# Kernel optimization log

Hardware: AMD Instinct MI355X
Metric: run time of the kernel (lower is better)

The kernel has to match this reference:

```python
import jax, jax.numpy as jnp
import numpy as np

B, Q, K, D, H = 16, 128, 128, 512, 512
NEG = -1e6


def setup_inputs() -> dict:
    key = jax.random.key(0)
    ks = jax.random.split(key, 7)
    return {
        "queries": jax.random.normal(ks[0], (B, Q, D), dtype=jnp.float32),
        "keys": jax.random.normal(ks[1], (B, K, D), dtype=jnp.float32),
        "values": jax.random.normal(ks[2], (B, K, D), dtype=jnp.float32),
        "valid_lens": jax.random.randint(ks[3], (B,), 1, K + 1, dtype=jnp.int32),
        "Wq": jax.random.normal(ks[4], (D, H), dtype=jnp.float32) / np.sqrt(D),
        "Wk": jax.random.normal(ks[5], (D, H), dtype=jnp.float32) / np.sqrt(D),
        "wv": jax.random.normal(ks[6], (H,), dtype=jnp.float32) / np.sqrt(H),
    }


def reference(queries, keys, values, valid_lens, Wq, Wk, wv):
    # projections (LazyLinear, bias=False)
    q = jnp.einsum("bqd,dh->bqh", queries, Wq)  # [B,Q,H]
    k = jnp.einsum("bkd,dh->bkh", keys, Wk)    # [B,K,H]
    # broadcast add -> tanh -> reduce to scalar score (Bahdanau)
    feats = jnp.tanh(q[:, :, None, :] + k[:, None, :, :])  # [B,Q,K,H]
    scores = jnp.einsum("bqkh,h->bqk", feats, wv)           # [B,Q,K]
    # masked softmax over key dim using per-batch valid lengths
    mask = jnp.arange(scores.shape[-1])[None, None, :] < valid_lens[:, None, None]
    scores = jnp.where(mask, scores, NEG)
    attn = jax.nn.softmax(scores, axis=-1)                  # [B,Q,K]
    # dropout is identity in eval mode
    return jnp.einsum("bqk,bkv->bqv", attn, values)
```

## Files before the change

kernel.cpp:

```cpp
#include <hip/hip_runtime.h>

#define Bn 16
#define Qn 128
#define Kn 128
#define Dn 512
#define Hn 512
#define NEGV (-3.0e38f)
#define PSCALE 2.8853900817779268f

typedef short s16x8 __attribute__((ext_vector_type(8)));
typedef float f32x4 __attribute__((ext_vector_type(4)));

__device__ __forceinline__ float exp2_hw(float x) {
  float r;
  asm("v_exp_f32 %0, %1" : "=v"(r) : "v"(x));
  return r;
}
__device__ __forceinline__ float rcp_hw(float x) { return __builtin_amdgcn_rcpf(x); }
__device__ __forceinline__ unsigned short f2bf(float f) {
  unsigned int u = __float_as_uint(f);
  u += 0x7fff + ((u >> 16) & 1);
  return (unsigned short)(u >> 16);
}
__device__ __forceinline__ unsigned int pack2bf(float lo, float hi) {
  return (unsigned int)f2bf(lo) | ((unsigned int)f2bf(hi) << 16);
}
__device__ __forceinline__ float bfl(unsigned int u) { return __uint_as_float(u << 16); }
__device__ __forceinline__ float bfh(unsigned int u) { return __uint_as_float(u & 0xffff0000u); }

__global__ __launch_bounds__(256) void convert_w(
    const float* __restrict__ Wq, const float* __restrict__ Wk,
    unsigned short* __restrict__ Wt)
{
  __shared__ float Tl[64][68];
  const int bid = blockIdx.x, t = threadIdx.x;
  const int sel = bid >> 6, tile = bid & 63;
  const int kt = tile >> 3, nt = tile & 7;
  const float* W = sel ? Wk : Wq;

  const int r0 = t >> 4, c4 = (t & 15) * 4;
  #pragma unroll
  for (int p = 0; p < 4; ++p) {
    int r = r0 + p * 16;
    float4 v = *(const float4*)(W + (size_t)(kt * 64 + r) * Hn + nt * 64 + c4);
    *(float4*)&Tl[r][c4] = v;
  }
  __syncthreads();

  const int n_l = t >> 3, k8 = (t & 7) * 8;
  #pragma unroll
  for (int p = 0; p < 2; ++p) {
    int n = n_l + p * 32;
    unsigned short o[8];
    #pragma unroll
    for (int i = 0; i < 8; ++i) o[i] = f2bf(Tl[k8 + i][n]);
    unsigned short* dst = Wt + (size_t)sel * 262144 + (size_t)(nt * 64 + n) * 512 + kt * 64 + k8;
    *(ushort4*)dst = *(const ushort4*)&o[0];
    *(ushort4*)(dst + 4) = *(const ushort4*)&o[4];
  }
}

__global__ __launch_bounds__(256) void proj_mfma(
    const float* __restrict__ queries, const float* __restrict__ keys,
    const unsigned short* __restrict__ Wt, const float* __restrict__ wv,
    unsigned int* __restrict__ QWp, unsigned int* __restrict__ Ekp)
{
  __shared__ unsigned short Al[64][72];
  __shared__ unsigned short Bl[128][72];
  __shared__ float Tep[64][68];
  const int t = threadIdx.x, w = t >> 6, l = t & 63;
  const int wm = w >> 1, wn = w & 1;
  const int rowTile = blockIdx.x;
  const int n0 = blockIdx.y * 128;
  const int R0 = rowTile * 64;
  const bool isQ = rowTile < 32;
  const float* Asrc = isQ ? queries : keys;
  const int rowBase = isQ ? R0 : (R0 - 2048);
  const unsigned short* Wsel = Wt + (isQ ? 0 : 262144);

  f32x4 acc[2][4];
  #pragma unroll
  for (int m = 0; m < 2; ++m)
    #pragma unroll
    for (int n = 0; n < 4; ++n) acc[m][n] = (f32x4)0.f;

  const int lr = l & 15, lk = l >> 4;

  for (int k0 = 0; k0 < Hn; k0 += 64) {
    float4 afr[4];
    ushort4 br[4][2];
    #pragma unroll
    for (int i = 0; i < 4; ++i) {
      int g = t + 256 * i, r = g >> 4, c4 = g & 15;
      afr[i] = *(const float4*)(Asrc + (size_t)(rowBase + r) * Dn + k0 + c4 * 4);
    }
    #pragma unroll
    for (int i = 0; i < 4; ++i) {
      int g = t + 256 * i, r = g >> 3, c = g & 7;
      const unsigned short* p = Wsel + (size_t)(n0 + r) * Hn + k0 + c * 8;
      br[i][0] = *(const ushort4*)p; br[i][1] = *(const ushort4*)(p + 4);
    }
    __syncthreads();
    #pragma unroll
    for (int i = 0; i < 4; ++i) {
      int g = t + 256 * i, r = g >> 4, c4 = g & 15;
      ushort4 o = {f2bf(afr[i].x), f2bf(afr[i].y), f2bf(afr[i].z), f2bf(afr[i].w)};
      *(ushort4*)&Al[r][c4 * 4] = o;
    }
    #pragma unroll
    for (int i = 0; i < 4; ++i) {
      int g = t + 256 * i, r = g >> 3, c = g & 7;
      *(ushort4*)&Bl[r][c * 8] = br[i][0]; *(ushort4*)&Bl[r][c * 8 + 4] = br[i][1];
    }
    __syncthreads();
    #pragma unroll
    for (int ks = 0; ks < 2; ++ks) {
      s16x8 af[2], bf_[4];
      #pragma unroll
      for (int m = 0; m < 2; ++m)
        af[m] = *(const s16x8*)&Al[wm * 32 + m * 16 + lr][ks * 32 + lk * 8];
      #pragma unroll
      for (int n = 0; n < 4; ++n)
        bf_[n] = *(const s16x8*)&Bl[wn * 64 + n * 16 + lr][ks * 32 + lk * 8];
      #pragma unroll
      for (int m = 0; m < 2; ++m)
        #pragma unroll
        for (int n = 0; n < 4; ++n)
          acc[m][n] = __builtin_amdgcn_mfma_f32_16x16x32_bf16(af[m], bf_[n], acc[m][n], 0, 0, 0);
    }
    __syncthreads();
  }

  if (isQ) {
    #pragma unroll
    for (int m = 0; m < 2; ++m)
      #pragma unroll
      for (int n = 0; n < 4; ++n)
        #pragma unroll
        for (int r = 0; r < 4; ++r) {
          int row = R0 + wm * 32 + m * 16 + lk * 4 + r;
          int col = n0 + wn * 64 + n * 16 + lr;
          float a = acc[m][n][r];
          float F  = exp2_hw(-PSCALE * a);
          float WF = -2.f * wv[col] * F;
          QWp[(size_t)row * Hn + col] = pack2bf(WF, F);
        }
  } else {
    const int krow0 = R0 - 2048;
    const int bb = krow0 >> 7, kb = krow0 & 127;
    const int hl = t >> 2, kq = (t & 3) * 16;
    #pragma unroll
    for (int hc = 0; hc < 2; ++hc) {
      __syncthreads();
      if (wn == hc) {
        #pragma unroll
        for (int m = 0; m < 2; ++m)
          #pragma unroll
          for (int n = 0; n < 4; ++n)
            #pragma unroll
            for (int r = 0; r < 4; ++r) {
              int row_l = wm * 32 + m * 16 + lk * 4 + r;
              int h_l = n * 16 + lr;
              Tep[h_l][row_l] = exp2_hw(PSCALE * acc[m][n][r]);
            }
      }
      __syncthreads();
      unsigned int* dst = Ekp + (size_t)bb * 32768
                        + (size_t)(n0 + hc * 64 + hl) * 64 + (kb + kq) / 2;
      #pragma unroll
      for (int j = 0; j < 4; ++j) {
        float4 v = *(const float4*)&Tep[hl][kq + j * 4];
        uint2 o = {pack2bf(v.x, v.y), pack2bf(v.z, v.w)};
        *(uint2*)(dst + j * 2) = o;
      }
    }
  }
}

__device__ __forceinline__ void term8(float WF0, float F0, float WF1, float F1,
                                      const float ek0[8], const float ek1[8],
                                      float acc[8]) {
  #pragma unroll
  for (int j = 0; j < 8; ++j) {
    float d0 = F0 + ek0[j];
    float d1 = F1 + ek1[j];
    float num = __builtin_fmaf(WF0, d1, WF1 * d0);
    acc[j] = __builtin_fmaf(num, rcp_hw(d0 * d1), acc[j]);
  }
}

__global__ __launch_bounds__(256) void score_kernel(
    const unsigned int* __restrict__ QWp, const unsigned int* __restrict__ Ekp,
    float* __restrict__ Sp)
{
  __shared__ float EkL[64][128];
  __shared__ unsigned int QWLu[32][68];
  const int id = blockIdx.x;
  const int g = id & 127, qt = id >> 7;
  const int b = g >> 3, hs = g & 7;
  const int t = threadIdx.x, w = t >> 6, l = t & 63;
  const int qp = w * 8 + ((l >> 4) << 1);
  const int ka8 = (l & 15) * 8;

  {
    const uint4* esrc = (const uint4*)(Ekp + (size_t)b * 32768 + (size_t)hs * 4096);
    uint4 er[4];
    #pragma unroll
    for (int i = 0; i < 4; ++i) er[i] = esrc[t + 256 * i];
    uint4 qr[2];
    #pragma unroll
    for (int i = 0; i < 2; ++i) {
      int lin = t + 256 * i, row = lin >> 4, c4 = lin & 15;
      qr[i] = *(const uint4*)(QWp + (size_t)(b * Qn + qt * 32 + row) * Hn + hs * 64 + c4 * 4);
    }
    #pragma unroll
    for (int i = 0; i < 4; ++i) {
      int lin = t + 256 * i, row = lin >> 4, c4 = lin & 15;
      const unsigned int u[4] = {er[i].x, er[i].y, er[i].z, er[i].w};
      float f[8];
      #pragma unroll
      for (int p = 0; p < 4; ++p) { f[2 * p] = bfl(u[p]); f[2 * p + 1] = bfh(u[p]); }
      *(float4*)&EkL[row][c4 * 8]     = *(const float4*)&f[0];
      *(float4*)&EkL[row][c4 * 8 + 4] = *(const float4*)&f[4];
    }
    #pragma unroll
    for (int i = 0; i < 2; ++i) {
      int lin = t + 256 * i, row = lin >> 4, c4 = lin & 15;
      *(uint4*)&QWLu[row][c4 * 4] = qr[i];
    }
  }
  __syncthreads();

  float acc0[8], acc1[8];
  #pragma unroll
  for (int j = 0; j < 8; ++j) { acc0[j] = 0.f; acc1[j] = 0.f; }

  #pragma unroll 4
  for (int hb = 0; hb < 32; ++hb) {
    float ek0[8], ek1[8];
    *(float4*)&ek0[0] = *(const float4*)&EkL[2 * hb][ka8];
    *(float4*)&ek0[4] = *(const float4*)&EkL[2 * hb][ka8 + 4];
    *(float4*)&ek1[0] = *(const float4*)&EkL[2 * hb + 1][ka8];
    *(float4*)&ek1[4] = *(const float4*)&EkL[2 * hb + 1][ka8 + 4];
    uint2 qa = *(const uint2*)&QWLu[qp][hb * 2];
    uint2 qb = *(const uint2*)&QWLu[qp + 1][hb * 2];
    term8(bfl(qa.x), bfh(qa.x), bfl(qa.y), bfh(qa.y), ek0, ek1, acc0);
    term8(bfl(qb.x), bfh(qb.x), bfl(qb.y), bfh(qb.y), ek0, ek1, acc1);
  }

  const int q = qt * 32 + qp;
  size_t sb = (((size_t)hs * Bn + b) * Qn + q) * Kn;
  *(float4*)(Sp + sb + ka8)          = (float4){acc0[0], acc0[1], acc0[2], acc0[3]};
  *(float4*)(Sp + sb + ka8 + 4)      = (float4){acc0[4], acc0[5], acc0[6], acc0[7]};
  *(float4*)(Sp + sb + Kn + ka8)     = (float4){acc1[0], acc1[1], acc1[2], acc1[3]};
  *(float4*)(Sp + sb + Kn + ka8 + 4) = (float4){acc1[4], acc1[5], acc1[6], acc1[7]};
}

__global__ __launch_bounds__(256) void softmax_av(
    const float* __restrict__ Sp, const int* __restrict__ valid_lens,
    const float* __restrict__ values, float* __restrict__ out)
{
  __shared__ unsigned short AtL[16][136];
  __shared__ unsigned int VLu[128][36];
  const int t = threadIdx.x, w = t >> 6, l = t & 63;
  const int b = blockIdx.y;
  const int qt = blockIdx.x & 7;
  const int dt = blockIdx.x >> 3;
  const int lr = l & 15, lk = l >> 4;

  {
    const int q_l = t >> 4, k8 = (t & 15) * 8;
    const size_t base = ((size_t)(b * Qn) + qt * 16 + q_l) * Kn + k8;
    float s[8] = {0.f, 0.f, 0.f, 0.f, 0.f, 0.f, 0.f, 0.f};
    #pragma unroll
    for (int p = 0; p < 8; ++p) {
      float4 a0 = *(const float4*)(Sp + base + (size_t)p * 262144);
      float4 a1 = *(const float4*)(Sp + base + (size_t)p * 262144 + 4);
      s[0] += a0.x; s[1] += a0.y; s[2] += a0.z; s[3] += a0.w;
      s[4] += a1.x; s[5] += a1.y; s[6] += a1.z; s[7] += a1.w;
    }
    const int vlen = valid_lens[b];
    bool ok[8];
    float m = NEGV;
    #pragma unroll
    for (int j = 0; j < 8; ++j) {
      ok[j] = (k8 + j) < vlen;
      if (ok[j]) m = fmaxf(m, s[j]);
    }
    #pragma unroll
    for (int xm = 8; xm >= 1; xm >>= 1) m = fmaxf(m, __shfl_xor(m, xm));
    float e[8], sum = 0.f;
    #pragma unroll
    for (int j = 0; j < 8; ++j) {
      e[j] = ok[j] ? exp2_hw((s[j] - m) * 1.44269504f) : 0.f;
      sum += e[j];
    }
    #pragma unroll
    for (int xm = 8; xm >= 1; xm >>= 1) sum += __shfl_xor(sum, xm);
    float inv = rcp_hw(sum);
    ushort4 o0 = {f2bf(e[0] * inv), f2bf(e[1] * inv), f2bf(e[2] * inv), f2bf(e[3] * inv)};
    ushort4 o1 = {f2bf(e[4] * inv), f2bf(e[5] * inv), f2bf(e[6] * inv), f2bf(e[7] * inv)};
    *(ushort4*)&AtL[q_l][k8] = o0;
    *(ushort4*)&AtL[q_l][k8 + 4] = o1;
  }
  __syncthreads();

  const int kread = t & 15, dread = (t >> 4) & 15;
  f32x4 acc[2];
  acc[0] = (f32x4)0.f; acc[1] = (f32x4)0.f;
  #pragma unroll
  for (int k0 = 0; k0 < Kn; k0 += 64) {
    if (k0) __syncthreads();
    #pragma unroll
    for (int j = 0; j < 4; ++j) {
      int k2 = kread + 16 * (j & 1);
      int d4 = dread + 16 * (j >> 1);
      const float* vp = values + ((size_t)(b * Kn) + k0 + 2 * k2) * Dn + dt * 128 + d4 * 4;
      float4 v0 = *(const float4*)(vp);
      float4 v1 = *(const float4*)(vp + Dn);
      VLu[d4 * 4 + 0][k2] = pack2bf(v0.x, v1.x);
      VLu[d4 * 4 + 1][k2] = pack2bf(v0.y, v1.y);
      VLu[d4 * 4 + 2][k2] = pack2bf(v0.z, v1.z);
      VLu[d4 * 4 + 3][k2] = pack2bf(v0.w, v1.w);
    }
    __syncthreads();
    #pragma unroll
    for (int ks = 0; ks < 2; ++ks) {
      s16x8 af = *(const s16x8*)&AtL[lr][k0 + ks * 32 + lk * 8];
      #pragma unroll
      for (int nn = 0; nn < 2; ++nn) {
        s16x8 bv = *(const s16x8*)&VLu[w * 32 + nn * 16 + lr][ks * 16 + lk * 4];
        acc[nn] = __builtin_amdgcn_mfma_f32_16x16x32_bf16(af, bv, acc[nn], 0, 0, 0);
      }
    }
  }
  #pragma unroll
  for (int nn = 0; nn < 2; ++nn)
    #pragma unroll
    for (int r = 0; r < 4; ++r) {
      int q = qt * 16 + lk * 4 + r;
      int d = dt * 128 + w * 32 + nn * 16 + lr;
      out[((size_t)(b * Qn) + q) * Dn + d] = acc[nn][r];
    }
}

extern "C" void kernel_launch(void* const* d_in, const int* in_sizes, int n_in,
                              void* d_out, int out_size, void* d_ws, size_t ws_size,
                              hipStream_t stream) {
  const float* queries    = (const float*)d_in[0];
  const float* keys       = (const float*)d_in[1];
  const float* values     = (const float*)d_in[2];
  const int*   valid_lens = (const int*)d_in[3];
  const float* Wq         = (const float*)d_in[4];
  const float* Wk         = (const float*)d_in[5];
  const float* wv         = (const float*)d_in[6];
  float* out = (float*)d_out;

  unsigned short* Wt  = (unsigned short*)d_ws;
  unsigned int*   QWp = (unsigned int*)(Wt + 524288);
  unsigned int*   Ekp = QWp + 1048576;
  float*          Sp  = (float*)(Ekp + 524288);

  convert_w<<<128, 256, 0, stream>>>(Wq, Wk, Wt);
  proj_mfma<<<dim3(64, 4), 256, 0, stream>>>(queries, keys, Wt, wv, QWp, Ekp);
  score_kernel<<<512, 256, 0, stream>>>(QWp, Ekp, Sp);
  softmax_av<<<dim3(32, 16), 256, 0, stream>>>(Sp, valid_lens, values, out);
}
```

Before: 46.19 us.

## Fuse score computation with masked softmax and attention-value matmul

Merges score_kernel and softmax_av into one kernel in which each 512-thread block handles 8 queries of one batch. The block loops over all 8 H-slices to accumulate full scores in registers, runs the softmax with wave-level shuffles, and feeds the probabilities to the MFMA value product. This removes the partial-score buffer written to global memory, its re-read, and one launch. In exchange there are only 256 blocks, each looping serially over H, half of every MFMA tile is zero padding, and each block re-reads Ek and the values tiles for its batch.

```diff
diff --git a/kernel.cpp b/kernel.cpp
--- a/kernel.cpp
+++ b/kernel.cpp
@@ -177,171 +177,122 @@
   }
 }
 
-__device__ __forceinline__ void term8(float WF0, float F0, float WF1, float F1,
-                                      const float ek0[8], const float ek1[8],
-                                      float acc[8]) {
-  #pragma unroll
-  for (int j = 0; j < 8; ++j) {
-    float d0 = F0 + ek0[j];
-    float d1 = F1 + ek1[j];
-    float num = __builtin_fmaf(WF0, d1, WF1 * d0);
-    acc[j] = __builtin_fmaf(num, rcp_hw(d0 * d1), acc[j]);
-  }
-}
-
-__global__ __launch_bounds__(256) void score_kernel(
+__global__ __launch_bounds__(512) void fused_sav(
     const unsigned int* __restrict__ QWp, const unsigned int* __restrict__ Ekp,
-    float* __restrict__ Sp)
+    const int* __restrict__ valid_lens, const float* __restrict__ values,
+    float* __restrict__ out)
 {
-  __shared__ float EkL[64][128];
-  __shared__ unsigned int QWLu[32][68];
+  __shared__ union {
+    struct { float EkL[64][128]; unsigned int QWLu[8][512]; } s;
+    struct { unsigned short AtL[16][136]; unsigned int VLu[128][36]; } a;
+  } sm;
   const int id = blockIdx.x;
-  const int g = id & 127, qt = id >> 7;
-  const int b = g >> 3, hs = g & 7;
-  const int t = threadIdx.x, w = t >> 6, l = t & 63;
-  const int qp = w * 8 + ((l >> 4) << 1);
-  const int ka8 = (l & 15) * 8;
-
-  {
-    const uint4* esrc = (const uint4*)(Ekp + (size_t)b * 32768 + (size_t)hs * 4096);
-    uint4 er[4];
-    #pragma unroll
-    for (int i = 0; i < 4; ++i) er[i] = esrc[t + 256 * i];
-    uint4 qr[2];
-    #pragma unroll
-    for (int i = 0; i < 2; ++i) {
-      int lin = t + 256 * i, row = lin >> 4, c4 = lin & 15;
-      qr[i] = *(const uint4*)(QWp + (size_t)(b * Qn + qt * 32 + row) * Hn + hs * 64 + c4 * 4);
-    }
-    #pragma unroll
-    for (int i = 0; i < 4; ++i) {
-      int lin = t + 256 * i, row = lin >> 4, c4 = lin & 15;
-      const unsigned int u[4] = {er[i].x, er[i].y, er[i].z, er[i].w};
-      float f[8];
-      #pragma unroll
-      for (int p = 0; p < 4; ++p) { f[2 * p] = bfl(u[p]); f[2 * p + 1] = bfh(u[p]); }
-      *(float4*)&EkL[row][c4 * 8]     = *(const float4*)&f[0];
-      *(float4*)&EkL[row][c4 * 8 + 4] = *(const float4*)&f[4];
-    }
-    #pragma unroll
-    for (int i = 0; i < 2; ++i) {
-      int lin = t + 256 * i, row = lin >> 4, c4 = lin & 15;
-      *(uint4*)&QWLu[row][c4 * 4] = qr[i];
-    }
-  }
+  const int b  = ((id & 7) << 1) | (id >> 7);
+  const int qt = (id >> 3) & 15;
+  const int t = threadIdx.x, l = t & 63, wq = t >> 6;
+  const int k2 = l * 2;
+  const int lr = l & 15, lk = l >> 4;
+
+  #pragma unroll
+  for (int i = 0; i < 2; ++i) {
+    int lin = t + 512 * i;
+    int row = lin >> 7, c4 = lin & 127;
+    uint4 v = *(const uint4*)(QWp + (size_t)(b * Qn + qt * 8 + row) * Hn + c4 * 4);
+    *(uint4*)&sm.s.QWLu[row][c4 * 4] = v;
+  }
+
+  float acc0 = 0.f, acc1 = 0.f;
+  for (int hs = 0; hs < 8; ++hs) {
+    __syncthreads();
+    {
+      const uint4* esrc = (const uint4*)(Ekp + (size_t)b * 32768 + (size_t)hs * 4096);
+      #pragma unroll
+      for (int i = 0; i < 2; ++i) {
+        int lin = t + 512 * i;
+        uint4 e = esrc[lin];
+        int row = lin >> 4, c4 = lin & 15;
+        const unsigned int u[4] = {e.x, e.y, e.z, e.w};
+        float f[8];
+        #pragma unroll
+        for (int p = 0; p < 4; ++p) { f[2 * p] = bfl(u[p]); f[2 * p + 1] = bfh(u[p]); }
+        *(float4*)&sm.s.EkL[row][c4 * 8]     = *(const float4*)&f[0];
+        *(float4*)&sm.s.EkL[row][c4 * 8 + 4] = *(const float4*)&f[4];
+      }
+    }
+    __syncthreads();
+    const unsigned int* qrow = &sm.s.QWLu[wq][hs * 64];
+    #pragma unroll 4
+    for (int hb = 0; hb < 32; ++hb) {
+      float2 e0 = *(const float2*)&sm.s.EkL[2 * hb][k2];
+      float2 e1 = *(const float2*)&sm.s.EkL[2 * hb + 1][k2];
+      uint2 qa = *(const uint2*)&qrow[hb * 2];
+      const float WF0 = bfl(qa.x), F0 = bfh(qa.x);
+      const float WF1 = bfl(qa.y), F1 = bfh(qa.y);
+      float d0, d1, num;
+      d0 = F0 + e0.x; d1 = F1 + e1.x;
+      num = __builtin_fmaf(WF0, d1, WF1 * d0);
+      acc0 = __builtin_fmaf(num, rcp_hw(d0 * d1), acc0);
+      d0 = F0 + e0.y; d1 = F1 + e1.y;
+      num = __builtin_fmaf(WF0, d1, WF1 * d0);
+      acc1 = __builtin_fmaf(num, rcp_hw(d0 * d1), acc1);
+    }
+  }
+
+  const int vlen = valid_lens[b];
+  const bool ok0 = k2 < vlen, ok1 = (k2 + 1) < vlen;
+  float m = fmaxf(ok0 ? acc0 : NEGV, ok1 ? acc1 : NEGV);
+  #pragma unroll
+  for (int xm = 32; xm >= 1; xm >>= 1) m = fmaxf(m, __shfl_xor(m, xm));
+  float e0v = ok0 ? exp2_hw((acc0 - m) * 1.44269504f) : 0.f;
+  float e1v = ok1 ? exp2_hw((acc1 - m) * 1.44269504f) : 0.f;
+  float ssum = e0v + e1v;
+  #pragma unroll
+  for (int xm = 32; xm >= 1; xm >>= 1) ssum += __shfl_xor(ssum, xm);
+  float inv = rcp_hw(ssum);
+
   __syncthreads();
-
-  float acc0[8], acc1[8];
-  #pragma unroll
-  for (int j = 0; j < 8; ++j) { acc0[j] = 0.f; acc1[j] = 0.f; }
-
-  #pragma unroll 4
-  for (int hb = 0; hb < 32; ++hb) {
-    float ek0[8], ek1[8];
-    *(float4*)&ek0[0] = *(const float4*)&EkL[2 * hb][ka8];
-    *(float4*)&ek0[4] = *(const float4*)&EkL[2 * hb][ka8 + 4];
-    *(float4*)&ek1[0] = *(const float4*)&EkL[2 * hb + 1][ka8];
-    *(float4*)&ek1[4] = *(const float4*)&EkL[2 * hb + 1][ka8 + 4];
-    uint2 qa = *(const uint2*)&QWLu[qp][hb * 2];
-    uint2 qb = *(const uint2*)&QWLu[qp + 1][hb * 2];
-    term8(bfl(qa.x), bfh(qa.x), bfl(qa.y), bfh(qa.y), ek0, ek1, acc0);
-    term8(bfl(qb.x), bfh(qb.x), bfl(qb.y), bfh(qb.y), ek0, ek1, acc1);
-  }
-
-  const int q = qt * 32 + qp;
-  size_t sb = (((size_t)hs * Bn + b) * Qn + q) * Kn;
-  *(float4*)(Sp + sb + ka8)          = (float4){acc0[0], acc0[1], acc0[2], acc0[3]};
-  *(float4*)(Sp + sb + ka8 + 4)      = (float4){acc0[4], acc0[5], acc0[6], acc0[7]};
-  *(float4*)(Sp + sb + Kn + ka8)     = (float4){acc1[0], acc1[1], acc1[2], acc1[3]};
-  *(float4*)(Sp + sb + Kn + ka8 + 4) = (float4){acc1[4], acc1[5], acc1[6], acc1[7]};
-}
-
-__global__ __launch_bounds__(256) void softmax_av(
-    const float* __restrict__ Sp, const int* __restrict__ valid_lens,
-    const float* __restrict__ values, float* __restrict__ out)
-{
-  __shared__ unsigned short AtL[16][136];
-  __shared__ unsigned int VLu[128][36];
-  const int t = threadIdx.x, w = t >> 6, l = t & 63;
-  const int b = blockIdx.y;
-  const int qt = blockIdx.x & 7;
-  const int dt = blockIdx.x >> 3;
-  const int lr = l & 15, lk = l >> 4;
-
-  {
-    const int q_l = t >> 4, k8 = (t & 15) * 8;
-    const size_t base = ((size_t)(b * Qn) + qt * 16 + q_l) * Kn + k8;
-    float s[8] = {0.f, 0.f, 0.f, 0.f, 0.f, 0.f, 0.f, 0.f};
-    #pragma unroll
-    for (int p = 0; p < 8; ++p) {
-      float4 a0 = *(const float4*)(Sp + base + (size_t)p * 262144);
-      float4 a1 = *(const float4*)(Sp + base + (size_t)p * 262144 + 4);
-      s[0] += a0.x; s[1] += a0.y; s[2] += a0.z; s[3] += a0.w;
-      s[4] += a1.x; s[5] += a1.y; s[6] += a1.z; s[7] += a1.w;
-    }
-    const int vlen = valid_lens[b];
-    bool ok[8];
-    float m = NEGV;
-    #pragma unroll
-    for (int j = 0; j < 8; ++j) {
-      ok[j] = (k8 + j) < vlen;
-      if (ok[j]) m = fmaxf(m, s[j]);
-    }
-    #pragma unroll
-    for (int xm = 8; xm >= 1; xm >>= 1) m = fmaxf(m, __shfl_xor(m, xm));
-    float e[8], sum = 0.f;
-    #pragma unroll
-    for (int j = 0; j < 8; ++j) {
-      e[j] = ok[j] ? exp2_hw((s[j] - m) * 1.44269504f) : 0.f;
-      sum += e[j];
-    }
-    #pragma unroll
-    for (int xm = 8; xm >= 1; xm >>= 1) sum += __shfl_xor(sum, xm);
-    float inv = rcp_hw(sum);
-    ushort4 o0 = {f2bf(e[0] * inv), f2bf(e[1] * inv), f2bf(e[2] * inv), f2bf(e[3] * inv)};
-    ushort4 o1 = {f2bf(e[4] * inv), f2bf(e[5] * inv), f2bf(e[6] * inv), f2bf(e[7] * inv)};
-    *(ushort4*)&AtL[q_l][k8] = o0;
-    *(ushort4*)&AtL[q_l][k8 + 4] = o1;
-  }
-  __syncthreads();
-
-  const int kread = t & 15, dread = (t >> 4) & 15;
-  f32x4 acc[2];
-  acc[0] = (f32x4)0.f; acc[1] = (f32x4)0.f;
-  #pragma unroll
-  for (int k0 = 0; k0 < Kn; k0 += 64) {
-    if (k0) __syncthreads();
-    #pragma unroll
-    for (int j = 0; j < 4; ++j) {
-      int k2 = kread + 16 * (j & 1);
-      int d4 = dread + 16 * (j >> 1);
-      const float* vp = values + ((size_t)(b * Kn) + k0 + 2 * k2) * Dn + dt * 128 + d4 * 4;
-      float4 v0 = *(const float4*)(vp);
-      float4 v1 = *(const float4*)(vp + Dn);
-      VLu[d4 * 4 + 0][k2] = pack2bf(v0.x, v1.x);
-      VLu[d4 * 4 + 1][k2] = pack2bf(v0.y, v1.y);
-      VLu[d4 * 4 + 2][k2] = pack2bf(v0.z, v1.z);
-      VLu[d4 * 4 + 3][k2] = pack2bf(v0.w, v1.w);
-    }
-    __syncthreads();
-    #pragma unroll
-    for (int ks = 0; ks < 2; ++ks) {
-      s16x8 af = *(const s16x8*)&AtL[lr][k0 + ks * 32 + lk * 8];
-      #pragma unroll
-      for (int nn = 0; nn < 2; ++nn) {
-        s16x8 bv = *(const s16x8*)&VLu[w * 32 + nn * 16 + lr][ks * 16 + lk * 4];
-        acc[nn] = __builtin_amdgcn_mfma_f32_16x16x32_bf16(af, bv, acc[nn], 0, 0, 0);
-      }
-    }
-  }
-  #pragma unroll
-  for (int nn = 0; nn < 2; ++nn)
+  sm.a.AtL[wq][k2]     = f2bf(e0v * inv);
+  sm.a.AtL[wq][k2 + 1] = f2bf(e1v * inv);
+  if (t < 128) {
+    int r8 = 8 + (t >> 4), c8 = (t & 15) * 8;
+    ushort4 z = {0, 0, 0, 0};
+    *(ushort4*)&sm.a.AtL[r8][c8] = z;
+    *(ushort4*)&sm.a.AtL[r8][c8 + 4] = z;
+  }
+
+  #pragma unroll
+  for (int dt = 0; dt < 4; ++dt) {
+    f32x4 acc = (f32x4)0.f;
+    #pragma unroll
+    for (int k0 = 0; k0 < Kn; k0 += 64) {
+      if (dt | k0) __syncthreads();
+      #pragma unroll
+      for (int j = 0; j < 2; ++j) {
+        int idx = t + 512 * j;
+        int k2v = idx & 31, d4 = (idx >> 5) & 31;
+        const float* vp = values + ((size_t)(b * Kn) + k0 + 2 * k2v) * Dn + dt * 128 + d4 * 4;
+        float4 v0 = *(const float4*)(vp);
+        float4 v1 = *(const float4*)(vp + Dn);
+        sm.a.VLu[d4 * 4 + 0][k2v] = pack2bf(v0.x, v1.x);
+        sm.a.VLu[d4 * 4 + 1][k2v] = pack2bf(v0.y, v1.y);
+        sm.a.VLu[d4 * 4 + 2][k2v] = pack2bf(v0.z, v1.z);
+        sm.a.VLu[d4 * 4 + 3][k2v] = pack2bf(v0.w, v1.w);
+      }
+      __syncthreads();
+      #pragma unroll
+      for (int ks = 0; ks < 2; ++ks) {
+        s16x8 af = *(const s16x8*)&sm.a.AtL[lr][k0 + ks * 32 + lk * 8];
+        s16x8 bv = *(const s16x8*)&sm.a.VLu[wq * 16 + lr][ks * 16 + lk * 4];
+        acc = __builtin_amdgcn_mfma_f32_16x16x32_bf16(af, bv, acc, 0, 0, 0);
+      }
+    }
     #pragma unroll
     for (int r = 0; r < 4; ++r) {
-      int q = qt * 16 + lk * 4 + r;
-      int d = dt * 128 + w * 32 + nn * 16 + lr;
-      out[((size_t)(b * Qn) + q) * Dn + d] = acc[nn][r];
-    }
+      int row = lk * 4 + r;
+      if (row < 8)
+        out[((size_t)(b * Qn) + qt * 8 + row) * Dn + dt * 128 + wq * 16 + lr] = acc[r];
+    }
+  }
 }
 
 extern "C" void kernel_launch(void* const* d_in, const int* in_sizes, int n_in,
@@ -359,10 +310,8 @@
   unsigned short* Wt  = (unsigned short*)d_ws;
   unsigned int*   QWp = (unsigned int*)(Wt + 524288);
   unsigned int*   Ekp = QWp + 1048576;
-  float*          Sp  = (float*)(Ekp + 524288);
 
   convert_w<<<128, 256, 0, stream>>>(Wq, Wk, Wt);
   proj_mfma<<<dim3(64, 4), 256, 0, stream>>>(queries, keys, Wt, wv, QWp, Ekp);
-  score_kernel<<<512, 256, 0, stream>>>(QWp, Ekp, Sp);
-  softmax_av<<<dim3(32, 16), 256, 0, stream>>>(Sp, valid_lens, values, out);
-}
+  fused_sav<<<256, 512, 0, stream>>>(QWp, Ekp, valid_lens, values, out);
+}
```

Result: slower. 68.17 us (+47.6%).
